# Optimization experiments

Measured on AMD Instinct MI355X. Metric: run time of the kernel, lower is better.

Reference implementation:

```python
import jax, jax.numpy as jnp
import numpy as np
from jax.scipy.linalg import block_diag

N_STATE, N_INPUT, HORIZON = 32, 16, 64


def setup_inputs() -> dict:
    key = jax.random.key(0)
    kA, kB, kC, kx = jax.random.split(key, 4)
    n_all = N_STATE + N_INPUT
    A = jax.random.normal(kA, (N_STATE, N_STATE), dtype=jnp.float32)
    B = jax.random.normal(kB, (N_STATE, N_INPUT), dtype=jnp.float32)
    Craw = jax.random.normal(kC, (HORIZON, n_all, n_all), dtype=jnp.float32)
    # symmetric positive-definite stage costs -> nonsingular KKT system
    C = jnp.einsum('tij,tkj->tik', Craw, Craw) / jnp.sqrt(jnp.float32(n_all)) \
        + jnp.eye(n_all, dtype=jnp.float32)
    x0 = jax.random.normal(kx, (N_STATE,), dtype=jnp.float32)
    return {"A": A, "B": B, "C": C, "T": HORIZON, "x0": x0}


def reference(A, B, C, T, x0):
    n_state = A.shape[0]
    n_input = B.shape[1]
    n_all = n_state + n_input
    dt = A.dtype

    # cost_mat: block-diagonal [n_all*T, n_all*T]
    cost_mat = block_diag(*C)

    # dynamics: [n_state*T, n_all*T]
    AB = jnp.concatenate((A, B), axis=1)              # [n_state, n_all]
    AB_blk = block_diag(*([AB] * (T - 1)))            # [(T-1)*n_state, (T-1)*n_all]
    dynamics = jnp.zeros((n_state * T, n_all * T), dtype=dt)
    dynamics = dynamics.at[:n_state, :n_state].set(jnp.eye(n_state, dtype=dt))
    dynamics = dynamics.at[n_state:n_state + (T - 1) * n_state,
                           :(T - 1) * n_all].set(AB_blk)
    # -I coupling entries: row n_state*t + i, col n_all*t + i, t=1..T-1
    t = jnp.arange(1, T)
    rows = (n_state * t)[:, None] + jnp.arange(n_state)[None, :]
    cols = (n_all * t)[:, None] + jnp.arange(n_state)[None, :]
    dynamics = dynamics.at[rows, cols].set(jnp.asarray(-1.0, dt))

    zero_mat = jnp.zeros((n_state * T, n_state * T), dtype=dt)
    full_mat = jnp.block([[cost_mat, dynamics.T],
                          [dynamics, zero_mat]])      # [(n_all+n_state)*T]^2

    # rhs: zeros except x0 at the start of the dynamics block
    sol = jnp.zeros(n_all * T + n_state * T, dtype=dt)
    sol = sol.at[n_all * T: n_all * T + n_state].set(x0)

    tau_mu = jnp.linalg.solve(full_mat, sol[:, None])[:, 0]
    tau_star = tau_mu[:n_all * T]
    mu_star = tau_mu[n_all * T:]
    return tau_star, mu_star
```

## Files before the change

kernel.cpp:

```cpp
#include <hip/hip_runtime.h>


namespace {

constexpr int NS  = 32;
constexpr int NI  = 16;
constexpr int NA  = 48;
constexpr int TT  = 64;
constexpr int NTH = 256;
constexpr int NBLK = 64;

using ull = unsigned long long;

__device__ __forceinline__ void fma4(float4& a, float s, const float4& b) {
  a.x += s * b.x; a.y += s * b.y; a.z += s * b.z; a.w += s * b.w;
}
__device__ __forceinline__ void fms4(float4& a, float s, const float4& b) {
  a.x -= s * b.x; a.y -= s * b.y; a.z -= s * b.z; a.w -= s * b.w;
}
__device__ __forceinline__ float dot4(const float4& a, const float4& b) {
  return a.x * b.x + a.y * b.y + a.z * b.z + a.w * b.w;
}
__device__ __forceinline__ float rdlane(float v, int l) {
  return __int_as_float(__builtin_amdgcn_readlane(__float_as_int(v), l));
}

__device__ __forceinline__ ull ald(const ull* p) {
  return __hip_atomic_load(p, __ATOMIC_RELAXED, __HIP_MEMORY_SCOPE_AGENT);
}
__device__ __forceinline__ void ast(ull* p, ull v) {
  __hip_atomic_store(p, v, __ATOMIC_RELAXED, __HIP_MEMORY_SCOPE_AGENT);
}
__device__ __forceinline__ float aldf(const float* p) {
  return __uint_as_float(__hip_atomic_load((const unsigned*)p,
      __ATOMIC_RELAXED, __HIP_MEMORY_SCOPE_AGENT));
}
__device__ __forceinline__ void astf(float* p, float v) {
  __hip_atomic_store((unsigned*)p, __float_as_uint(v),
      __ATOMIC_RELAXED, __HIP_MEMORY_SCOPE_AGENT);
}
__device__ __forceinline__ ull pack2(float x, float y) {
  return (ull)__float_as_uint(x) | ((ull)__float_as_uint(y) << 32);
}
__device__ __forceinline__ float2 unpack2(ull v) {
  return make_float2(__uint_as_float((unsigned)v),
                     __uint_as_float((unsigned)(v >> 32)));
}
__device__ __forceinline__ float4 ald4(const ull* p) {
  ull lo = ald(p), hi = ald(p + 1);
  float2 a = unpack2(lo), b = unpack2(hi);
  return make_float4(a.x, a.y, b.x, b.y);
}
__device__ __forceinline__ void ast4(ull* p, const float4& v) {
  ast(p, pack2(v.x, v.y)); ast(p + 1, pack2(v.z, v.w));
}

__device__ __forceinline__ unsigned fld(const unsigned* f) {
  return __hip_atomic_load(f, __ATOMIC_RELAXED, __HIP_MEMORY_SCOPE_AGENT);
}
__device__ __forceinline__ void fst(unsigned* f) {
  __hip_atomic_store(f, 1u, __ATOMIC_RELAXED, __HIP_MEMORY_SCOPE_AGENT);
}
__device__ __forceinline__ void waitf(const unsigned* f) {
  if (threadIdx.x == 0)
    while (fld(f) == 0) __builtin_amdgcn_s_sleep(1);
  __syncthreads();
}
__device__ __forceinline__ void setf(unsigned* f) {
  asm volatile("s_waitcnt vmcnt(0)" ::: "memory");
  __syncthreads();
  if (threadIdx.x == 0) fst(f);
}

template<int K>
__device__ __forceinline__ void tile_outer(const float* Acol0, int lda,
                                           const float* Bcol0, int ldb,
                                           float4 acc[4]) {
  #pragma unroll
  for (int m = 0; m < K; ++m) {
    const float4 va = *(const float4*)(Acol0 + m * lda);
    const float4 vb = *(const float4*)(Bcol0 + m * ldb);
    fma4(acc[0], va.x, vb); fma4(acc[1], va.y, vb);
    fma4(acc[2], va.z, vb); fma4(acc[3], va.w, vb);
  }
}

template<int KQ>
__device__ __forceinline__ void tile_dot(const float* Arow0, int lda,
                                         const float* Brow0, int ldb,
                                         float acc[4][4]) {
  #pragma unroll
  for (int q = 0; q < KQ; ++q) {
    float4 va[4], vb[4];
    #pragma unroll
    for (int r = 0; r < 4; ++r) va[r] = *(const float4*)(Arow0 + r * lda + 4 * q);
    #pragma unroll
    for (int c = 0; c < 4; ++c) vb[c] = *(const float4*)(Brow0 + c * ldb + 4 * q);
    #pragma unroll
    for (int r = 0; r < 4; ++r)
      #pragma unroll
      for (int c = 0; c < 4; ++c) acc[r][c] += dot4(va[r], vb[c]);
  }
}

__device__ __forceinline__ float step_dot(const float4 m[8], float x) {
  float a0 = 0.f, a1 = 0.f, a2 = 0.f, a3 = 0.f;
  #pragma unroll
  for (int q = 0; q < 8; ++q) {
    a0 += rdlane(x, 4 * q + 0) * m[q].x;
    a1 += rdlane(x, 4 * q + 1) * m[q].y;
    a2 += rdlane(x, 4 * q + 2) * m[q].z;
    a3 += rdlane(x, 4 * q + 3) * m[q].w;
  }
  return (a0 + a1) + (a2 + a3);
}

__global__ __launch_bounds__(NTH, 1) void lqr_all(
    const float* __restrict__ A, const float* __restrict__ Bm,
    const float* __restrict__ C, const float* __restrict__ x0,
    float* __restrict__ out,
    float* __restrict__ Sb0, float* __restrict__ Sb1,
    float* __restrict__ Mall, float* __restrict__ xs,
    unsigned* __restrict__ flg) {
  __shared__ float sC [NA][NA];
  __shared__ float sAB[NS][NA];
  __shared__ float sRi[NI][NI];
  __shared__ float sRiST[NS][NI];
  __shared__ float sBRi [NS][NI];
  __shared__ float sAi[NS][NS], sCi[NS][NS], sJi[NS][NS];
  __shared__ float sAj[NS][NS], sCj[NS][NS], sJj[NS][NS], sAjT[NS][NS];
  __shared__ float sT1[NS][NS], sT1T[NS][NS];
  __shared__ float sY1[NS][NS], sY2[NS][NS], sY3T[NS][NS], sW[NS][NS];
  __shared__ float sX[NS][NS], sZm[NS][NS];
  __shared__ float sP[NS][NS], sG[NS][NA], sFu[NI][NA], sK[NI][NS];
  __shared__ float sXt[NS];

  const int t = blockIdx.x, tid = threadIdx.x, lane = tid & 63, wid = tid >> 6;
  unsigned* wr = flg;
  unsigned* rd = flg + 448;
  unsigned* mf = flg + 832;
  unsigned* xf = flg + 896;

  {
    const float* Ct = C + (size_t)t * NA * NA;
    for (int e = tid; e < NA * NA; e += NTH) sC[e / NA][e % NA] = Ct[e];
    for (int e = tid; e < NS * NA; e += NTH) {
      int i = e / NA, j = e % NA;
      sAB[i][j] = (j < NS) ? A[i * NS + j] : Bm[i * NI + (j - NS)];
    }
    __syncthreads();
    if (wid == 0 && lane < 32) {
      const int c = lane;
      float f[NI];
      #pragma unroll
      for (int i = 0; i < NI; ++i)
        f[i] = (c < NI) ? sC[NS + i][NS + c] : ((c - NI) == i ? 1.f : 0.f);
      #pragma unroll
      for (int k = 0; k < NI; ++k) {
        float mi[NI];
        #pragma unroll
        for (int i = 0; i < NI; ++i) mi[i] = rdlane(f[i], k);
        const float inv = 1.0f / mi[k];
        f[k] *= inv;
        #pragma unroll
        for (int i = 0; i < NI; ++i) if (i != k) f[i] -= mi[i] * f[k];
      }
      if (c >= NI) {
        #pragma unroll
        for (int i = 0; i < NI; ++i) sRi[i][c - NI] = f[i];
      }
    }
    __syncthreads();
    if (tid < 32) {
      const int a = tid >> 2, b = tid & 3;
      float acc[4][4];
      #pragma unroll
      for (int r = 0; r < 4; ++r)
        #pragma unroll
        for (int c = 0; c < 4; ++c) acc[r][c] = 0.f;
      tile_dot<4>(&sC[4 * a][NS], NA, &sRi[4 * b][0], NI, acc);
      #pragma unroll
      for (int r = 0; r < 4; ++r)
        *(float4*)&sRiST[4 * a + r][4 * b] =
            make_float4(acc[r][0], acc[r][1], acc[r][2], acc[r][3]);
    } else if (tid < 64) {
      const int q = tid - 32, a = q >> 2, b = q & 3;
      float acc[4][4];
      #pragma unroll
      for (int r = 0; r < 4; ++r)
        #pragma unroll
        for (int c = 0; c < 4; ++c) acc[r][c] = 0.f;
      tile_dot<4>(&sAB[4 * a][NS], NA, &sRi[4 * b][0], NI, acc);
      #pragma unroll
      for (int r = 0; r < 4; ++r)
        *(float4*)&sBRi[4 * a + r][4 * b] =
            make_float4(acc[r][0], acc[r][1], acc[r][2], acc[r][3]);
    }
    __syncthreads();
    ull* outA = (ull*)(Sb0 + (size_t)t * 3072);
    ull* outC = outA + 512;
    ull* outJ = outA + 1024;
    if (tid < 64) {
      const int a = tid >> 3, b = tid & 7;
      float acc[4][4];
      #pragma unroll
      for (int r = 0; r < 4; ++r)
        #pragma unroll
        for (int c = 0; c < 4; ++c) acc[r][c] = 0.f;
      tile_dot<4>(&sRiST[4 * a][0], NI, &sC[4 * b][NS], NA, acc);
      #pragma unroll
      for (int r = 0; r < 4; ++r) {
        const float4 q4 = *(const float4*)&sC[4 * a + r][4 * b];
        const float4 v = make_float4(q4.x - acc[r][0], q4.y - acc[r][1],
                                     q4.z - acc[r][2], q4.w - acc[r][3]);
        *(float4*)&sJi[4 * a + r][4 * b] = v;
        ast4(outJ + ((4 * a + r) * NS + 4 * b) / 2, v);
      }
    } else if (tid < 128) {
      const int q = tid - 64, a = q >> 3, b = q & 7;
      float acc[4][4];
      #pragma unroll
      for (int r = 0; r < 4; ++r)
        #pragma unroll
        for (int c = 0; c < 4; ++c) acc[r][c] = 0.f;
      tile_dot<4>(&sBRi[4 * a][0], NI, &sC[4 * b][NS], NA, acc);
      #pragma unroll
      for (int r = 0; r < 4; ++r) {
        const float4 a4 = *(const float4*)&sAB[4 * a + r][4 * b];
        const float4 v = make_float4(a4.x - acc[r][0], a4.y - acc[r][1],
                                     a4.z - acc[r][2], a4.w - acc[r][3]);
        *(float4*)&sAi[4 * a + r][4 * b] = v;
        ast4(outA + ((4 * a + r) * NS + 4 * b) / 2, v);
      }
    } else if (tid < 192) {
      const int q = tid - 128, a = q >> 3, b = q & 7;
      float acc[4][4];
      #pragma unroll
      for (int r = 0; r < 4; ++r)
        #pragma unroll
        for (int c = 0; c < 4; ++c) acc[r][c] = 0.f;
      tile_dot<4>(&sBRi[4 * a][0], NI, &sAB[4 * b][NS], NA, acc);
      #pragma unroll
      for (int r = 0; r < 4; ++r) {
        const float4 v = make_float4(acc[r][0], acc[r][1], acc[r][2], acc[r][3]);
        *(float4*)&sCi[4 * a + r][4 * b] = v;
        ast4(outC + ((4 * a + r) * NS + 4 * b) / 2, v);
      }
    }
  }
  setf(&wr[0 * 64 + t]);

  for (int l = 0; l < 6; ++l) {
    const int off = 1 << l;
    const int rm = t + off;
    const float* Sin = (l & 1) ? Sb1 : Sb0;
    float* Sout = (l & 1) ? Sb0 : Sb1;
    ull* Eo = (ull*)(Sout + (size_t)t * 3072);
    if (rm >= TT) {
      if (l >= 1 && t >= (off >> 1)) waitf(&rd[(l - 1) * 64 + t]);
      ast(Eo + tid,        ((const ull*)sAi)[tid]);
      ast(Eo + 256 + tid,  ((const ull*)sAi)[tid + 256]);
      ast(Eo + 512 + tid,  ((const ull*)sCi)[tid]);
      ast(Eo + 768 + tid,  ((const ull*)sCi)[tid + 256]);
      ast(Eo + 1024 + tid, ((const ull*)sJi)[tid]);
      ast(Eo + 1280 + tid, ((const ull*)sJi)[tid + 256]);
    } else {
      waitf(&wr[l * 64 + rm]);
      const ull* Ej = (const ull*)(Sin + (size_t)rm * 3072);
      {
        ull r0 = ald(Ej + tid),        r1 = ald(Ej + 256 + tid);
        ull r2 = ald(Ej + 512 + tid),  r3 = ald(Ej + 768 + tid);
        ull r4 = ald(Ej + 1024 + tid), r5 = ald(Ej + 1280 + tid);
        ((ull*)sAj)[tid] = r0; ((ull*)sAj)[tid + 256] = r1;
        ((ull*)sCj)[tid] = r2; ((ull*)sCj)[tid + 256] = r3;
        ((ull*)sJj)[tid] = r4; ((ull*)sJj)[tid + 256] = r5;
      }
      __syncthreads();
      if (tid == 0) fst(&rd[l * 64 + rm]);
      #pragma unroll
      for (int r = 0; r < 4; ++r) {
        const int e = tid + 256 * r, i = e >> 5, j = e & 31;
        sAjT[j][i] = sAj[i][j];
      }
      if (tid < 64) {
        const int a = tid >> 3, b = tid & 7;
        float4 acc[4] = {make_float4(0,0,0,0), make_float4(0,0,0,0),
                         make_float4(0,0,0,0), make_float4(0,0,0,0)};
        tile_outer<NS>(&sCi[0][4 * a], NS, &sJj[0][4 * b], NS, acc);
        if (a == b) { acc[0].x += 1.f; acc[1].y += 1.f; acc[2].z += 1.f; acc[3].w += 1.f; }
        #pragma unroll
        for (int r = 0; r < 4; ++r) *(float4*)&sX[4 * a + r][4 * b] = acc[r];
      }
      __syncthreads();
      if (wid == 0) {
        const int c = lane;
        float f[NS];
        #pragma unroll
        for (int i = 0; i < NS; ++i)
          f[i] = (c < NS) ? sX[i][c] : ((c - NS) == i ? 1.f : 0.f);
        #pragma unroll
        for (int k = 0; k < NS; ++k) {
          float mi[NS];
          #pragma unroll
          for (int i = 0; i < NS; ++i) mi[i] = rdlane(f[i], k);
          const float inv = 1.0f / mi[k];
          f[k] *= inv;
          #pragma unroll
          for (int i = 0; i < NS; ++i) if (i != k) f[i] -= mi[i] * f[k];
        }
        if (c >= NS) {
          const int col = c - NS;
          #pragma unroll
          for (int i = 0; i < NS; ++i) sT1[i][col] = f[i];
          #pragma unroll
          for (int q = 0; q < 8; ++q)
            *(float4*)&sT1T[col][4 * q] =
                make_float4(f[4 * q], f[4 * q + 1], f[4 * q + 2], f[4 * q + 3]);
        }
      }
      __syncthreads();
      if (tid < 192) {
        const int grp = tid >> 6, q = tid & 63, a = q >> 3, b = q & 7;
        float4 acc[4] = {make_float4(0,0,0,0), make_float4(0,0,0,0),
                         make_float4(0,0,0,0), make_float4(0,0,0,0)};
        if (grp == 0) {
          tile_outer<NS>(&sT1T[0][4 * a], NS, &sAi[0][4 * b], NS, acc);
          #pragma unroll
          for (int r = 0; r < 4; ++r) *(float4*)&sY1[4 * a + r][4 * b] = acc[r];
        } else if (grp == 1) {
          tile_outer<NS>(&sT1T[0][4 * a], NS, &sCi[0][4 * b], NS, acc);
          #pragma unroll
          for (int r = 0; r < 4; ++r) *(float4*)&sY2[4 * a + r][4 * b] = acc[r];
        } else {
          tile_outer<NS>(&sT1[0][4 * a], NS, &sJj[0][4 * b], NS, acc);
          #pragma unroll
          for (int r = 0; r < 4; ++r) *(float4*)&sY3T[4 * a + r][4 * b] = acc[r];
        }
      }
      __syncthreads();
      if (tid < 192) {
        const int grp = tid >> 6, q = tid & 63, a = q >> 3, b = q & 7;
        float4 acc[4] = {make_float4(0,0,0,0), make_float4(0,0,0,0),
                         make_float4(0,0,0,0), make_float4(0,0,0,0)};
        if (grp == 0) {
          tile_outer<NS>(&sAjT[0][4 * a], NS, &sY1[0][4 * b], NS, acc);
          #pragma unroll
          for (int r = 0; r < 4; ++r) *(float4*)&sX[4 * a + r][4 * b] = acc[r];
        } else if (grp == 1) {
          tile_outer<NS>(&sAjT[0][4 * a], NS, &sY2[0][4 * b], NS, acc);
          #pragma unroll
          for (int r = 0; r < 4; ++r) *(float4*)&sZm[4 * a + r][4 * b] = acc[r];
        } else {
          tile_outer<NS>(&sY3T[0][4 * a], NS, &sAi[0][4 * b], NS, acc);
          #pragma unroll
          for (int r = 0; r < 4; ++r) *(float4*)&sW[4 * a + r][4 * b] = acc[r];
        }
      }
      __syncthreads();
      if (tid < 64) {
        const int a = tid >> 3, b = tid & 7;
        float acc[4][4];
        #pragma unroll
        for (int r = 0; r < 4; ++r)
          #pragma unroll
          for (int c = 0; c < 4; ++c) acc[r][c] = 0.f;
        tile_dot<8>(&sZm[4 * a][0], NS, &sAj[4 * b][0], NS, acc);
        #pragma unroll
        for (int r = 0; r < 4; ++r) {
          const float4 c4 = *(const float4*)&sCj[4 * a + r][4 * b];
          *(float4*)&sY2[4 * a + r][4 * b] =
              make_float4(acc[r][0] + c4.x, acc[r][1] + c4.y,
                          acc[r][2] + c4.z, acc[r][3] + c4.w);
        }
      } else if (tid < 128) {
        const int q = tid - 64, a = q >> 3, b = q & 7;
        float4 acc[4] = {make_float4(0,0,0,0), make_float4(0,0,0,0),
                         make_float4(0,0,0,0), make_float4(0,0,0,0)};
        tile_outer<NS>(&sAi[0][4 * a], NS, &sW[0][4 * b], NS, acc);
        #pragma unroll
        for (int r = 0; r < 4; ++r) {
          const float4 j4 = *(const float4*)&sJi[4 * a + r][4 * b];
          acc[r].x += j4.x; acc[r].y += j4.y; acc[r].z += j4.z; acc[r].w += j4.w;
          *(float4*)&sY1[4 * a + r][4 * b] = acc[r];
        }
      }
      __syncthreads();
      if (l >= 1 && t >= (off >> 1)) waitf(&rd[(l - 1) * 64 + t]);
      {
        ull x0_ = ((const ull*)sX)[tid],  x1_ = ((const ull*)sX)[tid + 256];
        ull y0_ = ((const ull*)sY2)[tid], y1_ = ((const ull*)sY2)[tid + 256];
        ull z0_ = ((const ull*)sY1)[tid], z1_ = ((const ull*)sY1)[tid + 256];
        ast(Eo + tid, x0_);        ast(Eo + 256 + tid, x1_);
        ast(Eo + 512 + tid, y0_);  ast(Eo + 768 + tid, y1_);
        ast(Eo + 1024 + tid, z0_); ast(Eo + 1280 + tid, z1_);
        ((ull*)sAi)[tid] = x0_; ((ull*)sAi)[tid + 256] = x1_;
        ((ull*)sCi)[tid] = y0_; ((ull*)sCi)[tid + 256] = y1_;
        ((ull*)sJi)[tid] = z0_; ((ull*)sJi)[tid + 256] = z1_;
      }
    }
    setf(&wr[(l + 1) * 64 + t]);
  }

  {
    for (int e = tid; e < NS * NA; e += NTH) {
      int i = e / NA, j = e % NA;
      sAB[i][j] = (j < NS) ? A[i * NS + j] : Bm[i * NI + (j - NS)];
    }
    const int ui = tid / 12, uk = tid - 12 * ui;
    float4 cr0 = make_float4(0,0,0,0), cr1 = make_float4(0,0,0,0);
    float4 cr2 = make_float4(0,0,0,0), cr3 = make_float4(0,0,0,0);
    if (tid < 48) {
      const float* Ct = C + (size_t)t * NA * NA;
      cr0 = *(const float4*)&Ct[(NS + 4 * ui + 0) * NA + 4 * uk];
      cr1 = *(const float4*)&Ct[(NS + 4 * ui + 1) * NA + 4 * uk];
      cr2 = *(const float4*)&Ct[(NS + 4 * ui + 2) * NA + 4 * uk];
      cr3 = *(const float4*)&Ct[(NS + 4 * ui + 3) * NA + 4 * uk];
    }
    if (t == TT - 1) {
      ((float4*)sP)[tid] = make_float4(0.f, 0.f, 0.f, 0.f);
    } else {
      waitf(&wr[6 * 64 + t + 1]);
      const ull* j64 = (const ull*)(Sb0 + (size_t)(t + 1) * 3072) + 1024;
      ((ull*)sP)[tid] = ald(j64 + tid);
      ((ull*)sP)[tid + 256] = ald(j64 + 256 + tid);
    }
    __syncthreads();
    if (tid < 96) {
      const int gi = tid / 12, gk = tid - 12 * gi;
      float4 acc[4] = {make_float4(0,0,0,0), make_float4(0,0,0,0),
                       make_float4(0,0,0,0), make_float4(0,0,0,0)};
      tile_outer<NS>(&sP[0][4 * gi], NS, &sAB[0][4 * gk], NA, acc);
      #pragma unroll
      for (int r = 0; r < 4; ++r) *(float4*)&sG[4 * gi + r][4 * gk] = acc[r];
    }
    __syncthreads();
    if (tid < 48) {
      float4 acc[4] = {cr0, cr1, cr2, cr3};
      tile_outer<NS>(&sAB[0][NS + 4 * ui], NA, &sG[0][4 * uk], NA, acc);
      #pragma unroll
      for (int r = 0; r < 4; ++r) *(float4*)&sFu[4 * ui + r][4 * uk] = acc[r];
    }
    __syncthreads();
    if (wid == 0) {
      const int col = (lane < 16) ? (NS + lane) : (lane - 16);
      float f[NI];
      #pragma unroll
      for (int i = 0; i < NI; ++i) f[i] = sFu[i][col];
      #pragma unroll
      for (int k = 0; k < NI; ++k) {
        float mi[NI];
        #pragma unroll
        for (int i = 0; i < NI; ++i) mi[i] = rdlane(f[i], k);
        const float inv = 1.0f / mi[k];
        f[k] *= inv;
        #pragma unroll
        for (int i = 0; i < NI; ++i) if (i != k) f[i] -= mi[i] * f[k];
      }
      if (lane >= 16 && lane < 48) {
        const int b = lane - 16;
        #pragma unroll
        for (int i = 0; i < NI; ++i) sK[i][b] = f[i];
      }
    }
    __syncthreads();
    if (tid < 64) {
      const int ma = tid >> 3, mb = tid & 7;
      float4 a0 = *(const float4*)&sAB[4 * ma + 0][4 * mb];
      float4 a1 = *(const float4*)&sAB[4 * ma + 1][4 * mb];
      float4 a2 = *(const float4*)&sAB[4 * ma + 2][4 * mb];
      float4 a3 = *(const float4*)&sAB[4 * ma + 3][4 * mb];
      #pragma unroll
      for (int q = 0; q < 4; ++q) {
        const float4 vf0 = *(const float4*)&sAB[4 * ma + 0][NS + 4 * q];
        const float4 vf1 = *(const float4*)&sAB[4 * ma + 1][NS + 4 * q];
        const float4 vf2 = *(const float4*)&sAB[4 * ma + 2][NS + 4 * q];
        const float4 vf3 = *(const float4*)&sAB[4 * ma + 3][NS + 4 * q];
        #pragma unroll
        for (int d = 0; d < 4; ++d) {
          const float4 vkk = *(const float4*)&sK[4 * q + d][4 * mb];
          const float s0 = (d == 0) ? vf0.x : (d == 1) ? vf0.y : (d == 2) ? vf0.z : vf0.w;
          const float s1 = (d == 0) ? vf1.x : (d == 1) ? vf1.y : (d == 2) ? vf1.z : vf1.w;
          const float s2 = (d == 0) ? vf2.x : (d == 1) ? vf2.y : (d == 2) ? vf2.z : vf2.w;
          const float s3 = (d == 0) ? vf3.x : (d == 1) ? vf3.y : (d == 2) ? vf3.z : vf3.w;
          fms4(a0, s0, vkk); fms4(a1, s1, vkk); fms4(a2, s2, vkk); fms4(a3, s3, vkk);
        }
      }
      ull* Mt = (ull*)(Mall + (size_t)t * NS * NS);
      ast4(Mt + (4 * ma + 0) * 16 + 2 * mb, a0);
      ast4(Mt + (4 * ma + 1) * 16 + 2 * mb, a1);
      ast4(Mt + (4 * ma + 2) * 16 + 2 * mb, a2);
      ast4(Mt + (4 * ma + 3) * 16 + 2 * mb, a3);
    }
  }
  setf(&mf[t]);

  if (t == 0) {
    if (tid < NBLK) {
      while (fld(&mf[tid]) == 0) __builtin_amdgcn_s_sleep(1);
    }
    __syncthreads();
    if (wid == 0) {
      const int i = lane;
      if (i < NS) {
        const ull* Mg = (const ull*)Mall;
        float4 mA[8], mB[8];
        float x = x0[i];
        out[i] = x; astf(&xs[i], x);
        #pragma unroll
        for (int q = 0; q < 8; ++q) mA[q] = ald4(Mg + 0 * 512 + i * 16 + 2 * q);
        #pragma unroll
        for (int q = 0; q < 8; ++q) mB[q] = ald4(Mg + 1 * 512 + i * 16 + 2 * q);
        for (int s = 0; s < TT - 1; s += 2) {
          x = step_dot(mA, x);
          out[(s + 1) * NA + i] = x; astf(&xs[(s + 1) * NS + i], x);
          if (s + 2 < TT - 1) {
            #pragma unroll
            for (int q = 0; q < 8; ++q) mA[q] = ald4(Mg + (s + 2) * 512 + i * 16 + 2 * q);
          }
          if (s + 1 < TT - 1) {
            x = step_dot(mB, x);
            out[(s + 2) * NA + i] = x; astf(&xs[(s + 2) * NS + i], x);
            if (s + 3 < TT - 1) {
              #pragma unroll
              for (int q = 0; q < 8; ++q) mB[q] = ald4(Mg + (s + 3) * 512 + i * 16 + 2 * q);
            }
          }
        }
      }
    }
    setf(xf);
  }
  waitf(xf);

  {
    if (tid < NS) sXt[tid] = aldf(&xs[(size_t)t * NS + tid]);
    __syncthreads();
    if (tid < NI) {
      const float4* Kr = (const float4*)&sK[tid][0];
      const float4* xr = (const float4*)sXt;
      float acc = 0.f;
      #pragma unroll
      for (int q = 0; q < 8; ++q) acc += dot4(Kr[q], xr[q]);
      out[t * NA + NS + tid] = -acc;
    } else if (tid < NI + NS) {
      const int i = tid - NI;
      const float4* Pr = (const float4*)&sJi[i][0];
      const float4* xr = (const float4*)sXt;
      float acc = 0.f;
      #pragma unroll
      for (int q = 0; q < 8; ++q) acc += dot4(Pr[q], xr[q]);
      out[NA * TT + t * NS + i] = (t == 0) ? -acc : acc;
    }
  }
}

}

extern "C" void kernel_launch(void* const* d_in, const int* in_sizes, int n_in,
                              void* d_out, int out_size, void* d_ws, size_t ws_size,
                              hipStream_t stream) {
  const float* A  = (const float*)d_in[0];
  const float* Bm = (const float*)d_in[1];
  const float* C  = (const float*)d_in[2];
  const float* x0 = (const float*)d_in[4];
  float* out = (float*)d_out;

  float* Sb0 = (float*)d_ws;
  float* Sb1 = Sb0 + (size_t)TT * 3072;
  float* Mall = Sb1 + (size_t)TT * 3072;
  float* xs   = Mall + (size_t)TT * NS * NS;
  unsigned* flg = (unsigned*)(xs + (size_t)TT * NS);

  hipMemsetAsync(flg, 0, 4096, stream);
  hipLaunchKernelGGL(lqr_all, dim3(NBLK), dim3(NTH), 0, stream,
                     A, Bm, C, x0, out, Sb0, Sb1, Mall, xs, flg);
}
```

Before: 143.3 us.

## Switch parallel Riccati scan to radix-4 and compute gains from own block's P

Replaces the six-level radix-2 doubling scan across blocks with a three-level radix-4 scan. Each block waits for and combines up to three partner elements per level, using a counter-based read acknowledgement in place of per-level flags. The gain/closed-loop computation is moved so block t computes K and M for stage t-1 from its own cost-to-go matrix. This removes the extra global wait and load of the neighbour's final result. The aim is to halve the number of grid-wide synchronisation rounds, at the cost of more sequential combines per level and more shared memory.

```diff
diff --git a/kernel.cpp b/kernel.cpp
--- a/kernel.cpp
+++ b/kernel.cpp
@@ -115,6 +115,10 @@
   return (a0 + a1) + (a2 + a3);
 }
 
+__device__ __forceinline__ int nlev4(int rm) {
+  return (rm < 48) ? 3 : (rm < 60) ? 2 : (rm < 63) ? 1 : 0;
+}
+
 __global__ __launch_bounds__(NTH, 1) void lqr_all(
     const float* __restrict__ A, const float* __restrict__ Bm,
     const float* __restrict__ C, const float* __restrict__ x0,
@@ -128,18 +132,19 @@
   __shared__ float sRiST[NS][NI];
   __shared__ float sBRi [NS][NI];
   __shared__ float sAi[NS][NS], sCi[NS][NS], sJi[NS][NS];
-  __shared__ float sAj[NS][NS], sCj[NS][NS], sJj[NS][NS], sAjT[NS][NS];
+  __shared__ float sAjs[3][NS][NS], sCjs[3][NS][NS], sJjs[3][NS][NS];
+  __shared__ float sAjT[NS][NS];
   __shared__ float sT1[NS][NS], sT1T[NS][NS];
   __shared__ float sY1[NS][NS], sY2[NS][NS], sY3T[NS][NS], sW[NS][NS];
   __shared__ float sX[NS][NS], sZm[NS][NS];
-  __shared__ float sP[NS][NS], sG[NS][NA], sFu[NI][NA], sK[NI][NS];
-  __shared__ float sXt[NS];
+  __shared__ float sG[NS][NA], sFu[NI][NA], sK[NI][NS], sK2[NI][NS];
+  __shared__ float sXt0[NS], sXt1[NS];
 
   const int t = blockIdx.x, tid = threadIdx.x, lane = tid & 63, wid = tid >> 6;
-  unsigned* wr = flg;
-  unsigned* rd = flg + 448;
-  unsigned* mf = flg + 832;
-  unsigned* xf = flg + 896;
+  unsigned* wr  = flg;
+  unsigned* rdc = flg + 256;
+  unsigned* mf  = flg + 448;
+  unsigned* xf  = flg + 512;
 
   {
     const float* Ct = C + (size_t)t * NA * NA;
@@ -250,188 +255,198 @@
   }
   setf(&wr[0 * 64 + t]);
 
-  for (int l = 0; l < 6; ++l) {
-    const int off = 1 << l;
-    const int rm = t + off;
-    const float* Sin = (l & 1) ? Sb1 : Sb0;
-    float* Sout = (l & 1) ? Sb0 : Sb1;
-    ull* Eo = (ull*)(Sout + (size_t)t * 3072);
-    if (rm >= TT) {
-      if (l >= 1 && t >= (off >> 1)) waitf(&rd[(l - 1) * 64 + t]);
-      ast(Eo + tid,        ((const ull*)sAi)[tid]);
-      ast(Eo + 256 + tid,  ((const ull*)sAi)[tid + 256]);
-      ast(Eo + 512 + tid,  ((const ull*)sCi)[tid]);
-      ast(Eo + 768 + tid,  ((const ull*)sCi)[tid + 256]);
-      ast(Eo + 1024 + tid, ((const ull*)sJi)[tid]);
-      ast(Eo + 1280 + tid, ((const ull*)sJi)[tid + 256]);
-    } else {
-      waitf(&wr[l * 64 + rm]);
-      const ull* Ej = (const ull*)(Sin + (size_t)rm * 3072);
-      {
-        ull r0 = ald(Ej + tid),        r1 = ald(Ej + 256 + tid);
-        ull r2 = ald(Ej + 512 + tid),  r3 = ald(Ej + 768 + tid);
-        ull r4 = ald(Ej + 1024 + tid), r5 = ald(Ej + 1280 + tid);
-        ((ull*)sAj)[tid] = r0; ((ull*)sAj)[tid + 256] = r1;
-        ((ull*)sCj)[tid] = r2; ((ull*)sCj)[tid + 256] = r3;
-        ((ull*)sJj)[tid] = r4; ((ull*)sJj)[tid + 256] = r5;
-      }
+  auto combine = [&](float (*Aj)[NS], float (*Cj)[NS], float (*Jj)[NS]) {
+    #pragma unroll
+    for (int r = 0; r < 4; ++r) {
+      const int e = tid + 256 * r, i = e >> 5, j = e & 31;
+      sAjT[j][i] = Aj[i][j];
+    }
+    if (tid < 64) {
+      const int a = tid >> 3, b = tid & 7;
+      float4 acc[4] = {make_float4(0,0,0,0), make_float4(0,0,0,0),
+                       make_float4(0,0,0,0), make_float4(0,0,0,0)};
+      tile_outer<NS>(&sCi[0][4 * a], NS, &Jj[0][4 * b], NS, acc);
+      if (a == b) { acc[0].x += 1.f; acc[1].y += 1.f; acc[2].z += 1.f; acc[3].w += 1.f; }
+      #pragma unroll
+      for (int r = 0; r < 4; ++r) *(float4*)&sX[4 * a + r][4 * b] = acc[r];
+    }
+    __syncthreads();
+    if (wid == 0) {
+      const int c = lane;
+      float f[NS];
+      #pragma unroll
+      for (int i = 0; i < NS; ++i)
+        f[i] = (c < NS) ? sX[i][c] : ((c - NS) == i ? 1.f : 0.f);
+      #pragma unroll
+      for (int k = 0; k < NS; ++k) {
+        float mi[NS];
+        #pragma unroll
+        for (int i = 0; i < NS; ++i) mi[i] = rdlane(f[i], k);
+        const float inv = 1.0f / mi[k];
+        f[k] *= inv;
+        #pragma unroll
+        for (int i = 0; i < NS; ++i) if (i != k) f[i] -= mi[i] * f[k];
+      }
+      if (c >= NS) {
+        const int col = c - NS;
+        #pragma unroll
+        for (int i = 0; i < NS; ++i) sT1[i][col] = f[i];
+        #pragma unroll
+        for (int q = 0; q < 8; ++q)
+          *(float4*)&sT1T[col][4 * q] =
+              make_float4(f[4 * q], f[4 * q + 1], f[4 * q + 2], f[4 * q + 3]);
+      }
+    }
+    __syncthreads();
+    if (tid < 192) {
+      const int grp = tid >> 6, q = tid & 63, a = q >> 3, b = q & 7;
+      float4 acc[4] = {make_float4(0,0,0,0), make_float4(0,0,0,0),
+                       make_float4(0,0,0,0), make_float4(0,0,0,0)};
+      if (grp == 0) {
+        tile_outer<NS>(&sT1T[0][4 * a], NS, &sAi[0][4 * b], NS, acc);
+        #pragma unroll
+        for (int r = 0; r < 4; ++r) *(float4*)&sY1[4 * a + r][4 * b] = acc[r];
+      } else if (grp == 1) {
+        tile_outer<NS>(&sT1T[0][4 * a], NS, &sCi[0][4 * b], NS, acc);
+        #pragma unroll
+        for (int r = 0; r < 4; ++r) *(float4*)&sY2[4 * a + r][4 * b] = acc[r];
+      } else {
+        tile_outer<NS>(&sT1[0][4 * a], NS, &Jj[0][4 * b], NS, acc);
+        #pragma unroll
+        for (int r = 0; r < 4; ++r) *(float4*)&sY3T[4 * a + r][4 * b] = acc[r];
+      }
+    }
+    __syncthreads();
+    if (tid < 192) {
+      const int grp = tid >> 6, q = tid & 63, a = q >> 3, b = q & 7;
+      float4 acc[4] = {make_float4(0,0,0,0), make_float4(0,0,0,0),
+                       make_float4(0,0,0,0), make_float4(0,0,0,0)};
+      if (grp == 0) {
+        tile_outer<NS>(&sAjT[0][4 * a], NS, &sY1[0][4 * b], NS, acc);
+        #pragma unroll
+        for (int r = 0; r < 4; ++r) *(float4*)&sX[4 * a + r][4 * b] = acc[r];
+      } else if (grp == 1) {
+        tile_outer<NS>(&sAjT[0][4 * a], NS, &sY2[0][4 * b], NS, acc);
+        #pragma unroll
+        for (int r = 0; r < 4; ++r) *(float4*)&sZm[4 * a + r][4 * b] = acc[r];
+      } else {
+        tile_outer<NS>(&sY3T[0][4 * a], NS, &sAi[0][4 * b], NS, acc);
+        #pragma unroll
+        for (int r = 0; r < 4; ++r) *(float4*)&sW[4 * a + r][4 * b] = acc[r];
+      }
+    }
+    __syncthreads();
+    if (tid < 64) {
+      const int a = tid >> 3, b = tid & 7;
+      float acc[4][4];
+      #pragma unroll
+      for (int r = 0; r < 4; ++r)
+        #pragma unroll
+        for (int c = 0; c < 4; ++c) acc[r][c] = 0.f;
+      tile_dot<8>(&sZm[4 * a][0], NS, &Aj[4 * b][0], NS, acc);
+      #pragma unroll
+      for (int r = 0; r < 4; ++r) {
+        const float4 c4 = *(const float4*)&Cj[4 * a + r][4 * b];
+        *(float4*)&sY2[4 * a + r][4 * b] =
+            make_float4(acc[r][0] + c4.x, acc[r][1] + c4.y,
+                        acc[r][2] + c4.z, acc[r][3] + c4.w);
+      }
+    } else if (tid < 128) {
+      const int q = tid - 64, a = q >> 3, b = q & 7;
+      float4 acc[4] = {make_float4(0,0,0,0), make_float4(0,0,0,0),
+                       make_float4(0,0,0,0), make_float4(0,0,0,0)};
+      tile_outer<NS>(&sAi[0][4 * a], NS, &sW[0][4 * b], NS, acc);
+      #pragma unroll
+      for (int r = 0; r < 4; ++r) {
+        const float4 j4 = *(const float4*)&sJi[4 * a + r][4 * b];
+        acc[r].x += j4.x; acc[r].y += j4.y; acc[r].z += j4.z; acc[r].w += j4.w;
+        *(float4*)&sY1[4 * a + r][4 * b] = acc[r];
+      }
+    }
+    __syncthreads();
+    ((ull*)sAi)[tid] = ((const ull*)sX)[tid];
+    ((ull*)sAi)[tid + 256] = ((const ull*)sX)[tid + 256];
+    ((ull*)sCi)[tid] = ((const ull*)sY2)[tid];
+    ((ull*)sCi)[tid + 256] = ((const ull*)sY2)[tid + 256];
+    ((ull*)sJi)[tid] = ((const ull*)sY1)[tid];
+    ((ull*)sJi)[tid + 256] = ((const ull*)sY1)[tid + 256];
+    __syncthreads();
+  };
+
+  for (int l = 0; l < 3; ++l) {
+    const int off = 1 << (2 * l);
+    if (t + off >= TT) break;
+    int nr = 0; int rms[3]; int vs[3];
+    #pragma unroll
+    for (int k = 1; k <= 3; ++k) {
+      const int rm = t + k * off;
+      if (rm < TT) {
+        rms[nr] = rm;
+        const int nl = nlev4(rm);
+        vs[nr] = (l < nl) ? l : nl;
+        ++nr;
+      }
+    }
+    if (tid == 0) {
+      for (int q = 0; q < nr; ++q)
+        while (fld(&wr[vs[q] * 64 + rms[q]]) == 0) __builtin_amdgcn_s_sleep(1);
+    }
+    __syncthreads();
+    for (int q = 0; q < nr; ++q) {
+      const float* Sin = (vs[q] & 1) ? Sb1 : Sb0;
+      const ull* Ej = (const ull*)(Sin + (size_t)rms[q] * 3072);
+      ull r0 = ald(Ej + tid),        r1 = ald(Ej + 256 + tid);
+      ull r2 = ald(Ej + 512 + tid),  r3 = ald(Ej + 768 + tid);
+      ull r4 = ald(Ej + 1024 + tid), r5 = ald(Ej + 1280 + tid);
+      ((ull*)sAjs[q])[tid] = r0; ((ull*)sAjs[q])[tid + 256] = r1;
+      ((ull*)sCjs[q])[tid] = r2; ((ull*)sCjs[q])[tid + 256] = r3;
+      ((ull*)sJjs[q])[tid] = r4; ((ull*)sJjs[q])[tid + 256] = r5;
+    }
+    __syncthreads();
+    if (tid == 0) {
+      for (int q = 0; q < nr; ++q)
+        if (vs[q] == l) atomicAdd(&rdc[l * 64 + rms[q]], 1u);
+    }
+    for (int q = 0; q < nr; ++q) combine(sAjs[q], sCjs[q], sJjs[q]);
+    if (l >= 1) {
+      const unsigned need = (3u < (unsigned)(t >> (2 * (l - 1))))
+                                ? 3u : (unsigned)(t >> (2 * (l - 1)));
+      if (tid == 0)
+        while (fld(&rdc[(l - 1) * 64 + t]) < need) __builtin_amdgcn_s_sleep(1);
       __syncthreads();
-      if (tid == 0) fst(&rd[l * 64 + rm]);
-      #pragma unroll
-      for (int r = 0; r < 4; ++r) {
-        const int e = tid + 256 * r, i = e >> 5, j = e & 31;
-        sAjT[j][i] = sAj[i][j];
-      }
-      if (tid < 64) {
-        const int a = tid >> 3, b = tid & 7;
-        float4 acc[4] = {make_float4(0,0,0,0), make_float4(0,0,0,0),
-                         make_float4(0,0,0,0), make_float4(0,0,0,0)};
-        tile_outer<NS>(&sCi[0][4 * a], NS, &sJj[0][4 * b], NS, acc);
-        if (a == b) { acc[0].x += 1.f; acc[1].y += 1.f; acc[2].z += 1.f; acc[3].w += 1.f; }
-        #pragma unroll
-        for (int r = 0; r < 4; ++r) *(float4*)&sX[4 * a + r][4 * b] = acc[r];
-      }
-      __syncthreads();
-      if (wid == 0) {
-        const int c = lane;
-        float f[NS];
-        #pragma unroll
-        for (int i = 0; i < NS; ++i)
-          f[i] = (c < NS) ? sX[i][c] : ((c - NS) == i ? 1.f : 0.f);
-        #pragma unroll
-        for (int k = 0; k < NS; ++k) {
-          float mi[NS];
-          #pragma unroll
-          for (int i = 0; i < NS; ++i) mi[i] = rdlane(f[i], k);
-          const float inv = 1.0f / mi[k];
-          f[k] *= inv;
-          #pragma unroll
-          for (int i = 0; i < NS; ++i) if (i != k) f[i] -= mi[i] * f[k];
-        }
-        if (c >= NS) {
-          const int col = c - NS;
-          #pragma unroll
-          for (int i = 0; i < NS; ++i) sT1[i][col] = f[i];
-          #pragma unroll
-          for (int q = 0; q < 8; ++q)
-            *(float4*)&sT1T[col][4 * q] =
-                make_float4(f[4 * q], f[4 * q + 1], f[4 * q + 2], f[4 * q + 3]);
-        }
-      }
-      __syncthreads();
-      if (tid < 192) {
-        const int grp = tid >> 6, q = tid & 63, a = q >> 3, b = q & 7;
-        float4 acc[4] = {make_float4(0,0,0,0), make_float4(0,0,0,0),
-                         make_float4(0,0,0,0), make_float4(0,0,0,0)};
-        if (grp == 0) {
-          tile_outer<NS>(&sT1T[0][4 * a], NS, &sAi[0][4 * b], NS, acc);
-          #pragma unroll
-          for (int r = 0; r < 4; ++r) *(float4*)&sY1[4 * a + r][4 * b] = acc[r];
-        } else if (grp == 1) {
-          tile_outer<NS>(&sT1T[0][4 * a], NS, &sCi[0][4 * b], NS, acc);
-          #pragma unroll
-          for (int r = 0; r < 4; ++r) *(float4*)&sY2[4 * a + r][4 * b] = acc[r];
-        } else {
-          tile_outer<NS>(&sT1[0][4 * a], NS, &sJj[0][4 * b], NS, acc);
-          #pragma unroll
-          for (int r = 0; r < 4; ++r) *(float4*)&sY3T[4 * a + r][4 * b] = acc[r];
-        }
-      }
-      __syncthreads();
-      if (tid < 192) {
-        const int grp = tid >> 6, q = tid & 63, a = q >> 3, b = q & 7;
-        float4 acc[4] = {make_float4(0,0,0,0), make_float4(0,0,0,0),
-                         make_float4(0,0,0,0), make_float4(0,0,0,0)};
-        if (grp == 0) {
-          tile_outer<NS>(&sAjT[0][4 * a], NS, &sY1[0][4 * b], NS, acc);
-          #pragma unroll
-          for (int r = 0; r < 4; ++r) *(float4*)&sX[4 * a + r][4 * b] = acc[r];
-        } else if (grp == 1) {
-          tile_outer<NS>(&sAjT[0][4 * a], NS, &sY2[0][4 * b], NS, acc);
-          #pragma unroll
-          for (int r = 0; r < 4; ++r) *(float4*)&sZm[4 * a + r][4 * b] = acc[r];
-        } else {
-          tile_outer<NS>(&sY3T[0][4 * a], NS, &sAi[0][4 * b], NS, acc);
-          #pragma unroll
-          for (int r = 0; r < 4; ++r) *(float4*)&sW[4 * a + r][4 * b] = acc[r];
-        }
-      }
-      __syncthreads();
-      if (tid < 64) {
-        const int a = tid >> 3, b = tid & 7;
-        float acc[4][4];
-        #pragma unroll
-        for (int r = 0; r < 4; ++r)
-          #pragma unroll
-          for (int c = 0; c < 4; ++c) acc[r][c] = 0.f;
-        tile_dot<8>(&sZm[4 * a][0], NS, &sAj[4 * b][0], NS, acc);
-        #pragma unroll
-        for (int r = 0; r < 4; ++r) {
-          const float4 c4 = *(const float4*)&sCj[4 * a + r][4 * b];
-          *(float4*)&sY2[4 * a + r][4 * b] =
-              make_float4(acc[r][0] + c4.x, acc[r][1] + c4.y,
-                          acc[r][2] + c4.z, acc[r][3] + c4.w);
-        }
-      } else if (tid < 128) {
-        const int q = tid - 64, a = q >> 3, b = q & 7;
-        float4 acc[4] = {make_float4(0,0,0,0), make_float4(0,0,0,0),
-                         make_float4(0,0,0,0), make_float4(0,0,0,0)};
-        tile_outer<NS>(&sAi[0][4 * a], NS, &sW[0][4 * b], NS, acc);
-        #pragma unroll
-        for (int r = 0; r < 4; ++r) {
-          const float4 j4 = *(const float4*)&sJi[4 * a + r][4 * b];
-          acc[r].x += j4.x; acc[r].y += j4.y; acc[r].z += j4.z; acc[r].w += j4.w;
-          *(float4*)&sY1[4 * a + r][4 * b] = acc[r];
-        }
-      }
-      __syncthreads();
-      if (l >= 1 && t >= (off >> 1)) waitf(&rd[(l - 1) * 64 + t]);
-      {
-        ull x0_ = ((const ull*)sX)[tid],  x1_ = ((const ull*)sX)[tid + 256];
-        ull y0_ = ((const ull*)sY2)[tid], y1_ = ((const ull*)sY2)[tid + 256];
-        ull z0_ = ((const ull*)sY1)[tid], z1_ = ((const ull*)sY1)[tid + 256];
-        ast(Eo + tid, x0_);        ast(Eo + 256 + tid, x1_);
-        ast(Eo + 512 + tid, y0_);  ast(Eo + 768 + tid, y1_);
-        ast(Eo + 1024 + tid, z0_); ast(Eo + 1280 + tid, z1_);
-        ((ull*)sAi)[tid] = x0_; ((ull*)sAi)[tid + 256] = x1_;
-        ((ull*)sCi)[tid] = y0_; ((ull*)sCi)[tid + 256] = y1_;
-        ((ull*)sJi)[tid] = z0_; ((ull*)sJi)[tid + 256] = z1_;
-      }
-    }
+    }
+    ull* Eo = (ull*)(((((l + 1) & 1)) ? Sb1 : Sb0) + (size_t)t * 3072);
+    ast(Eo + tid,        ((const ull*)sAi)[tid]);
+    ast(Eo + 256 + tid,  ((const ull*)sAi)[tid + 256]);
+    ast(Eo + 512 + tid,  ((const ull*)sCi)[tid]);
+    ast(Eo + 768 + tid,  ((const ull*)sCi)[tid + 256]);
+    ast(Eo + 1024 + tid, ((const ull*)sJi)[tid]);
+    ast(Eo + 1280 + tid, ((const ull*)sJi)[tid + 256]);
     setf(&wr[(l + 1) * 64 + t]);
   }
 
-  {
-    for (int e = tid; e < NS * NA; e += NTH) {
-      int i = e / NA, j = e % NA;
-      sAB[i][j] = (j < NS) ? A[i * NS + j] : Bm[i * NI + (j - NS)];
-    }
+  auto kmat = [&](int tau, bool hasP, float (*Pm)[NS], float (*Kd)[NS], bool wM) {
     const int ui = tid / 12, uk = tid - 12 * ui;
     float4 cr0 = make_float4(0,0,0,0), cr1 = make_float4(0,0,0,0);
     float4 cr2 = make_float4(0,0,0,0), cr3 = make_float4(0,0,0,0);
     if (tid < 48) {
-      const float* Ct = C + (size_t)t * NA * NA;
+      const float* Ct = C + (size_t)tau * NA * NA;
       cr0 = *(const float4*)&Ct[(NS + 4 * ui + 0) * NA + 4 * uk];
       cr1 = *(const float4*)&Ct[(NS + 4 * ui + 1) * NA + 4 * uk];
       cr2 = *(const float4*)&Ct[(NS + 4 * ui + 2) * NA + 4 * uk];
       cr3 = *(const float4*)&Ct[(NS + 4 * ui + 3) * NA + 4 * uk];
     }
-    if (t == TT - 1) {
-      ((float4*)sP)[tid] = make_float4(0.f, 0.f, 0.f, 0.f);
+    if (hasP) {
+      if (tid < 96) {
+        const int gi = tid / 12, gk = tid - 12 * gi;
+        float4 acc[4] = {make_float4(0,0,0,0), make_float4(0,0,0,0),
+                         make_float4(0,0,0,0), make_float4(0,0,0,0)};
+        tile_outer<NS>(&Pm[0][4 * gi], NS, &sAB[0][4 * gk], NA, acc);
+        #pragma unroll
+        for (int r = 0; r < 4; ++r) *(float4*)&sG[4 * gi + r][4 * gk] = acc[r];
+      }
     } else {
-      waitf(&wr[6 * 64 + t + 1]);
-      const ull* j64 = (const ull*)(Sb0 + (size_t)(t + 1) * 3072) + 1024;
-      ((ull*)sP)[tid] = ald(j64 + tid);
-      ((ull*)sP)[tid + 256] = ald(j64 + 256 + tid);
-    }
-    __syncthreads();
-    if (tid < 96) {
-      const int gi = tid / 12, gk = tid - 12 * gi;
-      float4 acc[4] = {make_float4(0,0,0,0), make_float4(0,0,0,0),
-                       make_float4(0,0,0,0), make_float4(0,0,0,0)};
-      tile_outer<NS>(&sP[0][4 * gi], NS, &sAB[0][4 * gk], NA, acc);
-      #pragma unroll
-      for (int r = 0; r < 4; ++r) *(float4*)&sG[4 * gi + r][4 * gk] = acc[r];
+      for (int e = tid; e < NS * NA; e += NTH) sG[e / NA][e % NA] = 0.f;
     }
     __syncthreads();
     if (tid < 48) {
@@ -459,11 +474,11 @@
       if (lane >= 16 && lane < 48) {
         const int b = lane - 16;
         #pragma unroll
-        for (int i = 0; i < NI; ++i) sK[i][b] = f[i];
-      }
-    }
-    __syncthreads();
-    if (tid < 64) {
+        for (int i = 0; i < NI; ++i) Kd[i][b] = f[i];
+      }
+    }
+    __syncthreads();
+    if (wM && tid < 64) {
       const int ma = tid >> 3, mb = tid & 7;
       float4 a0 = *(const float4*)&sAB[4 * ma + 0][4 * mb];
       float4 a1 = *(const float4*)&sAB[4 * ma + 1][4 * mb];
@@ -477,7 +492,7 @@
         const float4 vf3 = *(const float4*)&sAB[4 * ma + 3][NS + 4 * q];
         #pragma unroll
         for (int d = 0; d < 4; ++d) {
-          const float4 vkk = *(const float4*)&sK[4 * q + d][4 * mb];
+          const float4 vkk = *(const float4*)&Kd[4 * q + d][4 * mb];
           const float s0 = (d == 0) ? vf0.x : (d == 1) ? vf0.y : (d == 2) ? vf0.z : vf0.w;
           const float s1 = (d == 0) ? vf1.x : (d == 1) ? vf1.y : (d == 2) ? vf1.z : vf1.w;
           const float s2 = (d == 0) ? vf2.x : (d == 1) ? vf2.y : (d == 2) ? vf2.z : vf2.w;
@@ -485,13 +500,17 @@
           fms4(a0, s0, vkk); fms4(a1, s1, vkk); fms4(a2, s2, vkk); fms4(a3, s3, vkk);
         }
       }
-      ull* Mt = (ull*)(Mall + (size_t)t * NS * NS);
+      ull* Mt = (ull*)(Mall + (size_t)tau * NS * NS);
       ast4(Mt + (4 * ma + 0) * 16 + 2 * mb, a0);
       ast4(Mt + (4 * ma + 1) * 16 + 2 * mb, a1);
       ast4(Mt + (4 * ma + 2) * 16 + 2 * mb, a2);
       ast4(Mt + (4 * ma + 3) * 16 + 2 * mb, a3);
     }
-  }
+    __syncthreads();
+  };
+
+  if (t >= 1) kmat(t - 1, true, sJi, sK, true);
+  if (t == TT - 1) kmat(TT - 1, false, nullptr, sK2, false);
   setf(&mf[t]);
 
   if (t == 0) {
@@ -533,23 +552,33 @@
   waitf(xf);
 
   {
-    if (tid < NS) sXt[tid] = aldf(&xs[(size_t)t * NS + tid]);
-    __syncthreads();
-    if (tid < NI) {
+    if (tid < NS) sXt0[tid] = aldf(&xs[(size_t)t * NS + tid]);
+    else if (tid >= 64 && tid < 64 + NS && t >= 1)
+      sXt1[tid - 64] = aldf(&xs[(size_t)(t - 1) * NS + (tid - 64)]);
+    __syncthreads();
+    if (t >= 1 && tid < NI) {
       const float4* Kr = (const float4*)&sK[tid][0];
-      const float4* xr = (const float4*)sXt;
+      const float4* xr = (const float4*)sXt1;
       float acc = 0.f;
       #pragma unroll
       for (int q = 0; q < 8; ++q) acc += dot4(Kr[q], xr[q]);
-      out[t * NA + NS + tid] = -acc;
-    } else if (tid < NI + NS) {
+      out[(t - 1) * NA + NS + tid] = -acc;
+    } else if (tid >= NI && tid < NI + NS) {
       const int i = tid - NI;
       const float4* Pr = (const float4*)&sJi[i][0];
-      const float4* xr = (const float4*)sXt;
+      const float4* xr = (const float4*)sXt0;
       float acc = 0.f;
       #pragma unroll
       for (int q = 0; q < 8; ++q) acc += dot4(Pr[q], xr[q]);
       out[NA * TT + t * NS + i] = (t == 0) ? -acc : acc;
+    } else if (t == TT - 1 && tid >= 192 && tid < 192 + NI) {
+      const int i = tid - 192;
+      const float4* Kr = (const float4*)&sK2[i][0];
+      const float4* xr = (const float4*)sXt0;
+      float acc = 0.f;
+      #pragma unroll
+      for (int q = 0; q < 8; ++q) acc += dot4(Kr[q], xr[q]);
+      out[(TT - 1) * NA + NS + i] = -acc;
     }
   }
 }
```

After: 177.0 us. 23.5% more time.
